# Kernel optimization log

Measured on AMD Instinct MI355X. Metric: run time of the kernel, lower is better.

## Reference

```python
import jax, jax.numpy as jnp
import numpy as np

TOP_K = 2

def setup_inputs() -> dict:
    key = jax.random.key(0)
    ks = jax.random.split(key, 5)
    B, T, C, E, H = 4, 2048, 1024, 16, 4096
    x = jax.random.normal(ks[0], (B, T, C), dtype=jnp.float32)
    w_router = jax.random.normal(ks[1], (C, E), dtype=jnp.float32) / np.sqrt(C)
    w1 = jax.random.normal(ks[2], (E, C, H), dtype=jnp.float32) / np.sqrt(C)
    b1 = jnp.zeros((E, H), dtype=jnp.float32)
    w2 = jax.random.normal(ks[3], (E, H, C), dtype=jnp.float32) / np.sqrt(H)
    b2 = jnp.zeros((E, C), dtype=jnp.float32)
    return {"x": x, "w_router": w_router, "w1": w1, "b1": b1, "w2": w2, "b2": b2}


def reference(x, w_router, w1, b1, w2, b2):
    B, T, C = x.shape
    E = w1.shape[0]
    xf = x.reshape(-1, C)                       # [N, C]
    N = xf.shape[0]

    logits = xf @ w_router                      # [N, E]
    rw, sel = jax.lax.top_k(logits, TOP_K)      # [N, K]
    rw = jax.nn.softmax(rw.astype(jnp.float32), axis=-1).astype(x.dtype)

    # combine weight per (token, expert): sum of routing weights over the
    # k-slots that selected that expert (equivalent to the per-k masked loop)
    comb = jnp.zeros((N, E), dtype=x.dtype)
    comb = comb.at[jnp.arange(N)[:, None], sel].add(rw)  # [N, E]

    # loop over experts via scan: out += comb[:, e:e+1] * FFN_e(xf)
    def step(acc, params):
        w1e, b1e, w2e, b2e, ce = params         # ce: [N]
        h = jax.nn.relu(xf @ w1e + b1e)         # [N, 4C]
        y = h @ w2e + b2e                       # [N, C]
        return acc + ce[:, None] * y, None

    out0 = jnp.zeros_like(xf)
    out, _ = jax.lax.scan(step, out0, (w1, b1, w2, b2, comb.T))
    return out.reshape(B, T, C)
```

## Files before the change

### kernel.cpp

```cpp
#include <hip/hip_runtime.h>
#include <hip/hip_bf16.h>


typedef __attribute__((ext_vector_type(4))) float f32x4;
typedef __attribute__((ext_vector_type(8))) __bf16 bf16x8;
typedef __attribute__((ext_vector_type(8))) unsigned short u16x8;

#define NEXP 16
#define CAP  2048
#define CDIM 1024
#define HDIM 4096
#define BM 128
#define BN 128
#define BK 64
#define KS2 2

__device__ __forceinline__ unsigned short f2bf(float f) {
  return __builtin_bit_cast(unsigned short, (__bf16)f);
}

__device__ __forceinline__ int swz(int row, int b) {
  return row * (BK * 2) + (b ^ (((row >> 1) & 7) << 4));
}

typedef __attribute__((address_space(3))) void  lds_void;
typedef __attribute__((address_space(1))) const void gbl_void;
__device__ __forceinline__ void gload16(const void* g, void* l) {
  __builtin_amdgcn_global_load_lds((gbl_void*)g, (lds_void*)l, 16, 0, 0);
}

__device__ __forceinline__ void xcd_remap(int& bx, int& by, int& bz) {
  const int gx = gridDim.x, gy = gridDim.y;
  const int nwg = gx * gy * gridDim.z;
  int flat = blockIdx.x + gx * (blockIdx.y + gy * blockIdx.z);
  flat = (flat & 7) * (nwg >> 3) + (flat >> 3);
  bx = flat % gx;
  const int t = flat / gx;
  by = t % gy;
  bz = t / gy;
}

__global__ __launch_bounds__(64) void router_kernel(
    const float* __restrict__ x, const float* __restrict__ wr,
    float* __restrict__ pair_w, int* __restrict__ counts,
    int* __restrict__ lists)
{
  const int n = blockIdx.x;
  const int l = threadIdx.x;
  const float* xrow = x + (size_t)n * CDIM;
  double acc[NEXP];
#pragma unroll
  for (int e = 0; e < NEXP; e++) acc[e] = 0.0;
  for (int it = 0; it < CDIM / 64; it++) {
    const int c = l + it * 64;
    const double xv = (double)xrow[c];
    const float* w = wr + c * NEXP;
#pragma unroll
    for (int e = 0; e < NEXP; e++) acc[e] += xv * (double)w[e];
  }
#pragma unroll
  for (int e = 0; e < NEXP; e++) {
    double v = acc[e];
    for (int off = 32; off > 0; off >>= 1) v += __shfl_xor(v, off, 64);
    acc[e] = v;
  }
  if (l == 0) {
    int e0 = 0; double b0 = acc[0];
    for (int e = 1; e < NEXP; e++) if (acc[e] > b0) { b0 = acc[e]; e0 = e; }
    int e1 = -1; double b1v = -1e300;
    for (int e = 0; e < NEXP; e++) {
      if (e == e0) continue;
      if (acc[e] > b1v) { b1v = acc[e]; e1 = e; }
    }
    const double d = exp(b1v - b0);
    pair_w[2 * n]     = (float)(1.0 / (1.0 + d));
    pair_w[2 * n + 1] = (float)(d / (1.0 + d));
    int p0 = atomicAdd(&counts[e0], 1);
    if (p0 < CAP) lists[e0 * CAP + p0] = 2 * n;
    int p1 = atomicAdd(&counts[e1], 1);
    if (p1 < CAP) lists[e1 * CAP + p1] = 2 * n + 1;
  }
}

__global__ __launch_bounds__(256) void cvt_x_kernel(
    const float* __restrict__ x, unsigned short* __restrict__ xb, int n8)
{
  const int i = blockIdx.x * 256 + threadIdx.x;
  if (i >= n8) return;
  float4 a = ((const float4*)x)[2 * i];
  float4 b = ((const float4*)x)[2 * i + 1];
  u16x8 v;
  v[0] = f2bf(a.x); v[1] = f2bf(a.y); v[2] = f2bf(a.z); v[3] = f2bf(a.w);
  v[4] = f2bf(b.x); v[5] = f2bf(b.y); v[6] = f2bf(b.z); v[7] = f2bf(b.w);
  ((u16x8*)xb)[i] = v;
}

__global__ __launch_bounds__(256) void transpose_cvt_kernel(
    const float* __restrict__ src, unsigned short* __restrict__ dst,
    int K, int Nn)
{
  __shared__ __align__(16) unsigned short tile[64][72];
  const size_t eoff = (size_t)blockIdx.z * K * Nn;
  const float* S = src + eoff;
  unsigned short* D = dst + eoff;
  const int n0 = blockIdx.x * 64, k0 = blockIdx.y * 64;
  const int t = threadIdx.x;
  {
    const int nl = (t & 15) * 4, kr = t >> 4;
#pragma unroll
    for (int p = 0; p < 4; p++) {
      const int k = kr + p * 16;
      float4 v = *(const float4*)(S + (size_t)(k0 + k) * Nn + n0 + nl);
      tile[nl + 0][k] = f2bf(v.x);
      tile[nl + 1][k] = f2bf(v.y);
      tile[nl + 2][k] = f2bf(v.z);
      tile[nl + 3][k] = f2bf(v.w);
    }
  }
  __syncthreads();
  {
    const int kq = (t & 7) * 8, nr = t >> 3;
#pragma unroll
    for (int p = 0; p < 2; p++) {
      const int n = nr + p * 32;
      u16x8 v = *(const u16x8*)&tile[n][kq];
      *(u16x8*)(D + (size_t)(n0 + n) * K + k0 + kq) = v;
    }
  }
}

__global__ __launch_bounds__(256) void gemm1_async_kernel(
    const unsigned short* __restrict__ xb, const unsigned short* __restrict__ wb,
    const float* __restrict__ b1, const int* __restrict__ counts,
    const int* __restrict__ lists, unsigned short* __restrict__ Hb)
{
  int bx, by, bz;
  xcd_remap(bx, by, bz);
  const int e = bz;
  int cnt = counts[e]; if (cnt > CAP) cnt = CAP;
  const int m0 = by * BM;
  if (m0 >= cnt) return;
  const int n0 = bx * BN;
  const int* list = lists + e * CAP;
  const unsigned short* W = wb + (size_t)e * CDIM * HDIM;

  __shared__ __align__(16) unsigned short As[BM * BK];
  __shared__ __align__(16) unsigned short Bs[BN * BK];

  const int t = threadIdx.x, wid = t >> 6, lane = t & 63;
  const char* ag[4]; const char* bg[4];
  unsigned short* al[4]; unsigned short* bl[4];
#pragma unroll
  for (int i = 0; i < 4; i++) {
    const int r = wid * 32 + i * 8 + (lane >> 3);
    const int cb = ((lane & 7) ^ ((r >> 1) & 7)) << 4;
    int ai = m0 + r; if (ai > cnt - 1) ai = cnt - 1;
    const int tok = list[ai] >> 1;
    ag[i] = (const char*)(xb + (size_t)tok * CDIM) + cb;
    bg[i] = (const char*)(W + (size_t)(n0 + r) * CDIM) + cb;
    al[i] = As + (wid * 32 + i * 8) * BK;
    bl[i] = Bs + (wid * 32 + i * 8) * BK;
  }

  const int wm = (wid >> 1) * 64, wn = (wid & 1) * 64;
  const int lrow = lane & 15, lgrp = lane >> 4;
  f32x4 acc[4][4] = {};

  for (int kt = 0; kt < CDIM; kt += BK) {
#pragma unroll
    for (int i = 0; i < 4; i++) {
      gload16(ag[i] + kt * 2, al[i]);
      gload16(bg[i] + kt * 2, bl[i]);
    }
    __syncthreads();
#pragma unroll
    for (int kk = 0; kk < 2; kk++) {
      bf16x8 af[4], bfr[4];
      const int kb = (kk * 32 + lgrp * 8) * 2;
#pragma unroll
      for (int i = 0; i < 4; i++)
        af[i] = *(const bf16x8*)((const char*)As + swz(wm + i * 16 + lrow, kb));
#pragma unroll
      for (int j = 0; j < 4; j++)
        bfr[j] = *(const bf16x8*)((const char*)Bs + swz(wn + j * 16 + lrow, kb));
#pragma unroll
      for (int i = 0; i < 4; i++)
#pragma unroll
        for (int j = 0; j < 4; j++)
          acc[i][j] = __builtin_amdgcn_mfma_f32_16x16x32_bf16(af[i], bfr[j], acc[i][j], 0, 0, 0);
    }
    __syncthreads();
  }

  int hrow[4][4]; bool valid[4][4];
#pragma unroll
  for (int i = 0; i < 4; i++)
#pragma unroll
    for (int r = 0; r < 4; r++) {
      const int mi = m0 + wm + i * 16 + lgrp * 4 + r;
      valid[i][r] = (mi < cnt);
      hrow[i][r] = list[valid[i][r] ? mi : (cnt - 1)];
    }
#pragma unroll
  for (int j = 0; j < 4; j++) {
    const int col = n0 + wn + j * 16 + lrow;
    const float bias = b1[e * HDIM + col];
#pragma unroll
    for (int i = 0; i < 4; i++)
#pragma unroll
      for (int r = 0; r < 4; r++)
        if (valid[i][r]) {
          float h = acc[i][j][r] + bias;
          h = h > 0.f ? h : 0.f;
          Hb[(size_t)hrow[i][r] * HDIM + col] = f2bf(h);
        }
  }
}

__global__ __launch_bounds__(256) void gemm2_async_kernel(
    const unsigned short* __restrict__ Hb, const unsigned short* __restrict__ wb,
    const float* __restrict__ b2, const float* __restrict__ pair_w,
    const int* __restrict__ counts, const int* __restrict__ lists,
    float* __restrict__ out)
{
  int bx, by, bz;
  xcd_remap(bx, by, bz);
  const int e = bz / KS2, ks = bz % KS2;
  int cnt = counts[e]; if (cnt > CAP) cnt = CAP;
  const int m0 = by * BM;
  if (m0 >= cnt) return;
  const int n0 = bx * BN;
  const int* list = lists + e * CAP;
  const unsigned short* W = wb + (size_t)e * HDIM * CDIM;
  const int kbeg = ks * (HDIM / KS2), kend = kbeg + HDIM / KS2;

  __shared__ __align__(16) unsigned short As[BM * BK];
  __shared__ __align__(16) unsigned short Bs[BN * BK];

  const int t = threadIdx.x, wid = t >> 6, lane = t & 63;
  const char* ag[4]; const char* bg[4];
  unsigned short* al[4]; unsigned short* bl[4];
#pragma unroll
  for (int i = 0; i < 4; i++) {
    const int r = wid * 32 + i * 8 + (lane >> 3);
    const int cb = ((lane & 7) ^ ((r >> 1) & 7)) << 4;
    int ai = m0 + r; if (ai > cnt - 1) ai = cnt - 1;
    const int pr = list[ai];
    ag[i] = (const char*)(Hb + (size_t)pr * HDIM) + cb;
    bg[i] = (const char*)(W + (size_t)(n0 + r) * HDIM) + cb;
    al[i] = As + (wid * 32 + i * 8) * BK;
    bl[i] = Bs + (wid * 32 + i * 8) * BK;
  }

  const int wm = (wid >> 1) * 64, wn = (wid & 1) * 64;
  const int lrow = lane & 15, lgrp = lane >> 4;
  f32x4 acc[4][4] = {};

  for (int kt = kbeg; kt < kend; kt += BK) {
#pragma unroll
    for (int i = 0; i < 4; i++) {
      gload16(ag[i] + kt * 2, al[i]);
      gload16(bg[i] + kt * 2, bl[i]);
    }
    __syncthreads();
#pragma unroll
    for (int kk = 0; kk < 2; kk++) {
      bf16x8 af[4], bfr[4];
      const int kb = (kk * 32 + lgrp * 8) * 2;
#pragma unroll
      for (int i = 0; i < 4; i++)
        af[i] = *(const bf16x8*)((const char*)As + swz(wm + i * 16 + lrow, kb));
#pragma unroll
      for (int j = 0; j < 4; j++)
        bfr[j] = *(const bf16x8*)((const char*)Bs + swz(wn + j * 16 + lrow, kb));
#pragma unroll
      for (int i = 0; i < 4; i++)
#pragma unroll
        for (int j = 0; j < 4; j++)
          acc[i][j] = __builtin_amdgcn_mfma_f32_16x16x32_bf16(af[i], bfr[j], acc[i][j], 0, 0, 0);
    }
    __syncthreads();
  }

  float wgt[4][4]; int tok[4][4]; bool valid[4][4];
#pragma unroll
  for (int i = 0; i < 4; i++)
#pragma unroll
    for (int r = 0; r < 4; r++) {
      const int mi = m0 + wm + i * 16 + lgrp * 4 + r;
      valid[i][r] = (mi < cnt);
      const int p = list[valid[i][r] ? mi : (cnt - 1)];
      wgt[i][r] = pair_w[p];
      tok[i][r] = p >> 1;
    }
#pragma unroll
  for (int j = 0; j < 4; j++) {
    const int col = n0 + wn + j * 16 + lrow;
    const float bias = (ks == 0) ? b2[e * CDIM + col] : 0.f;
#pragma unroll
    for (int i = 0; i < 4; i++)
#pragma unroll
      for (int r = 0; r < 4; r++)
        if (valid[i][r])
          atomicAdd(out + (size_t)tok[i][r] * CDIM + col,
                    wgt[i][r] * (acc[i][j][r] + bias));
  }
}

__global__ __launch_bounds__(256) void gemm1_f32_kernel(
    const float* __restrict__ x, const float* __restrict__ w1,
    const float* __restrict__ b1, const int* __restrict__ counts,
    const int* __restrict__ lists, unsigned short* __restrict__ Hb,
    int e_base, int h_by_pair)
{
  const int e = e_base + blockIdx.z;
  int cnt = counts[e]; if (cnt > CAP) cnt = CAP;
  const int m0 = blockIdx.y * BM;
  if (m0 >= cnt) return;
  const int n0 = blockIdx.x * BN;
  const int* list = lists + e * CAP;
  const float* W = w1 + (size_t)e * CDIM * HDIM;
  __shared__ __align__(16) unsigned short As[BM * BK];
  __shared__ __align__(16) unsigned short Bs[BN * BK];
  const int t = threadIdx.x;
  const int a_row = t >> 1, a_half = t & 1;
  int a_idx = m0 + a_row; if (a_idx > cnt - 1) a_idx = cnt - 1;
  const float* a_src = x + (size_t)(list[a_idx] >> 1) * CDIM + a_half * 32;
  const int b_np = t & 63, b_kg = t >> 6;
  const int wid = t >> 6, lane = t & 63;
  const int wm = (wid >> 1) * 64, wn = (wid & 1) * 64;
  const int lrow = lane & 15, lgrp = lane >> 4;
  f32x4 acc[4][4] = {};
  for (int kt = 0; kt < CDIM; kt += BK) {
    {
      const float* s = a_src + kt;
      u16x8 cv[4];
#pragma unroll
      for (int q = 0; q < 4; q++) {
        float4 v0 = *(const float4*)(s + q * 8);
        float4 v1 = *(const float4*)(s + q * 8 + 4);
        cv[q][0] = f2bf(v0.x); cv[q][1] = f2bf(v0.y);
        cv[q][2] = f2bf(v0.z); cv[q][3] = f2bf(v0.w);
        cv[q][4] = f2bf(v1.x); cv[q][5] = f2bf(v1.y);
        cv[q][6] = f2bf(v1.z); cv[q][7] = f2bf(v1.w);
      }
#pragma unroll
      for (int q = 0; q < 4; q++)
        *(u16x8*)((char*)As + swz(a_row, (a_half * 32 + q * 8) * 2)) = cv[q];
    }
    {
#pragma unroll
      for (int it = 0; it < 2; it++) {
        const int k0 = (b_kg + 4 * it) * 8;
        u16x8 c0, c1;
#pragma unroll
        for (int j = 0; j < 8; j++) {
          float2 v = *(const float2*)(W + (size_t)(kt + k0 + j) * HDIM + n0 + 2 * b_np);
          c0[j] = f2bf(v.x); c1[j] = f2bf(v.y);
        }
        *(u16x8*)((char*)Bs + swz(2 * b_np,     k0 * 2)) = c0;
        *(u16x8*)((char*)Bs + swz(2 * b_np + 1, k0 * 2)) = c1;
      }
    }
    __syncthreads();
#pragma unroll
    for (int kk = 0; kk < 2; kk++) {
      bf16x8 af[4], bfr[4];
      const int kb = (kk * 32 + lgrp * 8) * 2;
#pragma unroll
      for (int i = 0; i < 4; i++)
        af[i] = *(const bf16x8*)((const char*)As + swz(wm + i * 16 + lrow, kb));
#pragma unroll
      for (int j = 0; j < 4; j++)
        bfr[j] = *(const bf16x8*)((const char*)Bs + swz(wn + j * 16 + lrow, kb));
#pragma unroll
      for (int i = 0; i < 4; i++)
#pragma unroll
        for (int j = 0; j < 4; j++)
          acc[i][j] = __builtin_amdgcn_mfma_f32_16x16x32_bf16(af[i], bfr[j], acc[i][j], 0, 0, 0);
    }
    __syncthreads();
  }
  int hrow[4][4]; bool valid[4][4];
#pragma unroll
  for (int i = 0; i < 4; i++)
#pragma unroll
    for (int r = 0; r < 4; r++) {
      const int mi = m0 + wm + i * 16 + lgrp * 4 + r;
      valid[i][r] = (mi < cnt);
      const int idx = valid[i][r] ? mi : (cnt - 1);
      hrow[i][r] = h_by_pair ? list[idx] : idx;
    }
#pragma unroll
  for (int j = 0; j < 4; j++) {
    const int col = n0 + wn + j * 16 + lrow;
    const float bias = b1[e * HDIM + col];
#pragma unroll
    for (int i = 0; i < 4; i++)
#pragma unroll
      for (int r = 0; r < 4; r++)
        if (valid[i][r]) {
          float h = acc[i][j][r] + bias;
          h = h > 0.f ? h : 0.f;
          Hb[(size_t)hrow[i][r] * HDIM + col] = f2bf(h);
        }
  }
}

__global__ __launch_bounds__(256) void gemm2_f32_kernel(
    const unsigned short* __restrict__ Hb, const float* __restrict__ w2,
    const float* __restrict__ b2, const float* __restrict__ pair_w,
    const int* __restrict__ counts, const int* __restrict__ lists,
    float* __restrict__ out, int e_base, int h_by_pair)
{
  const int e = e_base + blockIdx.z;
  int cnt = counts[e]; if (cnt > CAP) cnt = CAP;
  const int m0 = blockIdx.y * BM;
  if (m0 >= cnt) return;
  const int n0 = blockIdx.x * BN;
  const int* list = lists + e * CAP;
  const float* W = w2 + (size_t)e * HDIM * CDIM;
  __shared__ __align__(16) unsigned short As[BM * BK];
  __shared__ __align__(16) unsigned short Bs[BN * BK];
  const int t = threadIdx.x;
  const int a_row = t >> 1, a_half = t & 1;
  int a_idx = m0 + a_row; if (a_idx > cnt - 1) a_idx = cnt - 1;
  const unsigned short* a_src =
      Hb + (size_t)(h_by_pair ? list[a_idx] : a_idx) * HDIM + a_half * 32;
  const int b_np = t & 63, b_kg = t >> 6;
  const int wid = t >> 6, lane = t & 63;
  const int wm = (wid >> 1) * 64, wn = (wid & 1) * 64;
  const int lrow = lane & 15, lgrp = lane >> 4;
  f32x4 acc[4][4] = {};
  for (int kt = 0; kt < HDIM; kt += BK) {
    {
      const unsigned short* s = a_src + kt;
#pragma unroll
      for (int q = 0; q < 4; q++) {
        u16x8 v = *(const u16x8*)(s + q * 8);
        *(u16x8*)((char*)As + swz(a_row, (a_half * 32 + q * 8) * 2)) = v;
      }
    }
    {
#pragma unroll
      for (int it = 0; it < 2; it++) {
        const int k0 = (b_kg + 4 * it) * 8;
        u16x8 c0, c1;
#pragma unroll
        for (int j = 0; j < 8; j++) {
          float2 v = *(const float2*)(W + (size_t)(kt + k0 + j) * CDIM + n0 + 2 * b_np);
          c0[j] = f2bf(v.x); c1[j] = f2bf(v.y);
        }
        *(u16x8*)((char*)Bs + swz(2 * b_np,     k0 * 2)) = c0;
        *(u16x8*)((char*)Bs + swz(2 * b_np + 1, k0 * 2)) = c1;
      }
    }
    __syncthreads();
#pragma unroll
    for (int kk = 0; kk < 2; kk++) {
      bf16x8 af[4], bfr[4];
      const int kb = (kk * 32 + lgrp * 8) * 2;
#pragma unroll
      for (int i = 0; i < 4; i++)
        af[i] = *(const bf16x8*)((const char*)As + swz(wm + i * 16 + lrow, kb));
#pragma unroll
      for (int j = 0; j < 4; j++)
        bfr[j] = *(const bf16x8*)((const char*)Bs + swz(wn + j * 16 + lrow, kb));
#pragma unroll
      for (int i = 0; i < 4; i++)
#pragma unroll
        for (int j = 0; j < 4; j++)
          acc[i][j] = __builtin_amdgcn_mfma_f32_16x16x32_bf16(af[i], bfr[j], acc[i][j], 0, 0, 0);
    }
    __syncthreads();
  }
  float wgt[4][4]; int tok[4][4]; bool valid[4][4];
#pragma unroll
  for (int i = 0; i < 4; i++)
#pragma unroll
    for (int r = 0; r < 4; r++) {
      const int mi = m0 + wm + i * 16 + lgrp * 4 + r;
      valid[i][r] = (mi < cnt);
      const int idx = valid[i][r] ? mi : (cnt - 1);
      const int p = list[idx];
      wgt[i][r] = pair_w[p];
      tok[i][r] = p >> 1;
    }
#pragma unroll
  for (int j = 0; j < 4; j++) {
    const int col = n0 + wn + j * 16 + lrow;
    const float bias = b2[e * CDIM + col];
#pragma unroll
    for (int i = 0; i < 4; i++)
#pragma unroll
      for (int r = 0; r < 4; r++)
        if (valid[i][r])
          atomicAdd(out + (size_t)tok[i][r] * CDIM + col,
                    wgt[i][r] * (acc[i][j][r] + bias));
  }
}

extern "C" void kernel_launch(void* const* d_in, const int* in_sizes, int n_in,
                              void* d_out, int out_size, void* d_ws, size_t ws_size,
                              hipStream_t stream)
{
  const float* x  = (const float*)d_in[0];
  const float* wr = (const float*)d_in[1];
  const float* w1 = (const float*)d_in[2];
  const float* b1 = (const float*)d_in[3];
  const float* w2 = (const float*)d_in[4];
  const float* b2 = (const float*)d_in[5];
  float* out = (float*)d_out;

  const int N = in_sizes[0] / CDIM;

  char* ws = (char*)d_ws;
  int* counts = (int*)ws;
  int* lists  = (int*)(ws + 256);
  float* pw   = (float*)(ws + 256 + NEXP * CAP * 4);
  size_t off = 256 + (size_t)NEXP * CAP * 4 + (size_t)2 * N * 4;
  off = (off + 255) & ~(size_t)255;
  unsigned short* xb = (unsigned short*)(ws + off);
  const size_t xb_sz = (size_t)N * CDIM * 2;
  unsigned short* Hb = (unsigned short*)(ws + off + xb_sz);
  const size_t Hb_sz = (size_t)2 * N * HDIM * 2;
  unsigned short* wb = (unsigned short*)(ws + off + xb_sz + Hb_sz);
  const size_t wb_sz = (size_t)NEXP * CDIM * HDIM * 2;

  const size_t need_new = off + xb_sz + Hb_sz + wb_sz;
  const size_t need_old = off + Hb_sz;

  hipMemsetAsync(d_ws, 0, 64, stream);
  hipMemsetAsync(d_out, 0, (size_t)out_size * 4, stream);

  router_kernel<<<N, 64, 0, stream>>>(x, wr, pw, counts, lists);

  if (ws_size >= need_new) {
    cvt_x_kernel<<<(N * CDIM / 8 + 255) / 256, 256, 0, stream>>>(
        x, xb, N * CDIM / 8);
    transpose_cvt_kernel<<<dim3(HDIM / 64, CDIM / 64, NEXP), 256, 0, stream>>>(
        w1, wb, CDIM, HDIM);
    gemm1_async_kernel<<<dim3(HDIM / BN, CAP / BM, NEXP), 256, 0, stream>>>(
        xb, wb, b1, counts, lists, Hb);
    transpose_cvt_kernel<<<dim3(CDIM / 64, HDIM / 64, NEXP), 256, 0, stream>>>(
        w2, wb, HDIM, CDIM);
    gemm2_async_kernel<<<dim3(CDIM / BN, CAP / BM, NEXP * KS2), 256, 0, stream>>>(
        Hb, wb, b2, pw, counts, lists, out);
  } else if (ws_size >= need_old) {
    unsigned short* Hb0 = (unsigned short*)(ws + off);
    gemm1_f32_kernel<<<dim3(HDIM / BN, CAP / BM, NEXP), 256, 0, stream>>>(
        x, w1, b1, counts, lists, Hb0, 0, 1);
    gemm2_f32_kernel<<<dim3(CDIM / BN, CAP / BM, NEXP), 256, 0, stream>>>(
        Hb0, w2, b2, pw, counts, lists, out, 0, 1);
  }
}
```

Before: 1.088 ms.

## Double-buffer LDS tiles in async GEMM kernels to overlap loads with MFMA

The async bf16 GEMM kernels now keep two LDS buffers for the A and B tiles. Each iteration issues the global-to-LDS loads for the next K tile before computing the current one, then uses a partial vmcnt wait plus raw s_barrier in place of two __syncthreads. The goal is to hide global memory latency behind MFMA work. This doubles LDS use per block to 64KB, which may reduce occupancy, and it depends on the hand-written waitcnt counts being correct.

```diff
diff --git a/kernel.cpp b/kernel.cpp
--- a/kernel.cpp
+++ b/kernel.cpp
@@ -14,6 +14,7 @@
 #define BN 128
 #define BK 64
 #define KS2 2
+#define TILE_E (BM * BK)
 
 __device__ __forceinline__ unsigned short f2bf(float f) {
   return __builtin_bit_cast(unsigned short, (__bf16)f);
@@ -129,6 +130,25 @@
   }
 }
 
+#define MFMA_COMPUTE(Abase, Bbase)                                             \
+  _Pragma("unroll")                                                            \
+  for (int kk = 0; kk < 2; kk++) {                                             \
+    bf16x8 af[4], bfr[4];                                                      \
+    const int kb = (kk * 32 + lgrp * 8) * 2;                                   \
+    _Pragma("unroll")                                                          \
+    for (int i = 0; i < 4; i++)                                                \
+      af[i] = *(const bf16x8*)((Abase) + swz(wm + i * 16 + lrow, kb));         \
+    _Pragma("unroll")                                                          \
+    for (int j = 0; j < 4; j++)                                                \
+      bfr[j] = *(const bf16x8*)((Bbase) + swz(wn + j * 16 + lrow, kb));        \
+    _Pragma("unroll")                                                          \
+    for (int i = 0; i < 4; i++)                                                \
+      _Pragma("unroll")                                                        \
+      for (int j = 0; j < 4; j++)                                              \
+        acc[i][j] = __builtin_amdgcn_mfma_f32_16x16x32_bf16(                   \
+            af[i], bfr[j], acc[i][j], 0, 0, 0);                                \
+  }
+
 __global__ __launch_bounds__(256) void gemm1_async_kernel(
     const unsigned short* __restrict__ xb, const unsigned short* __restrict__ wb,
     const float* __restrict__ b1, const int* __restrict__ counts,
@@ -144,8 +164,8 @@
   const int* list = lists + e * CAP;
   const unsigned short* W = wb + (size_t)e * CDIM * HDIM;
 
-  __shared__ __align__(16) unsigned short As[BM * BK];
-  __shared__ __align__(16) unsigned short Bs[BN * BK];
+  __shared__ __align__(16) unsigned short As[2 * TILE_E];
+  __shared__ __align__(16) unsigned short Bs[2 * TILE_E];
 
   const int t = threadIdx.x, wid = t >> 6, lane = t & 63;
   const char* ag[4]; const char* bg[4];
@@ -166,30 +186,34 @@
   const int lrow = lane & 15, lgrp = lane >> 4;
   f32x4 acc[4][4] = {};
 
-  for (int kt = 0; kt < CDIM; kt += BK) {
+#pragma unroll
+  for (int i = 0; i < 4; i++) {
+    gload16(ag[i], al[i]);
+    gload16(bg[i], bl[i]);
+  }
+  const int NT = CDIM / BK;
+  for (int tt = 0; tt < NT - 1; ++tt) {
+    const int p = tt & 1;
+    const int koff = (tt + 1) * (BK * 2);
 #pragma unroll
     for (int i = 0; i < 4; i++) {
-      gload16(ag[i] + kt * 2, al[i]);
-      gload16(bg[i] + kt * 2, bl[i]);
-    }
-    __syncthreads();
-#pragma unroll
-    for (int kk = 0; kk < 2; kk++) {
-      bf16x8 af[4], bfr[4];
-      const int kb = (kk * 32 + lgrp * 8) * 2;
-#pragma unroll
-      for (int i = 0; i < 4; i++)
-        af[i] = *(const bf16x8*)((const char*)As + swz(wm + i * 16 + lrow, kb));
-#pragma unroll
-      for (int j = 0; j < 4; j++)
-        bfr[j] = *(const bf16x8*)((const char*)Bs + swz(wn + j * 16 + lrow, kb));
-#pragma unroll
-      for (int i = 0; i < 4; i++)
-#pragma unroll
-        for (int j = 0; j < 4; j++)
-          acc[i][j] = __builtin_amdgcn_mfma_f32_16x16x32_bf16(af[i], bfr[j], acc[i][j], 0, 0, 0);
-    }
-    __syncthreads();
+      gload16(ag[i] + koff, al[i] + (p ^ 1) * TILE_E);
+      gload16(bg[i] + koff, bl[i] + (p ^ 1) * TILE_E);
+    }
+    asm volatile("s_waitcnt vmcnt(8)" ::: "memory");
+    asm volatile("s_barrier" ::: "memory");
+    const char* Ab = (const char*)As + p * (TILE_E * 2);
+    const char* Bb = (const char*)Bs + p * (TILE_E * 2);
+    MFMA_COMPUTE(Ab, Bb)
+    asm volatile("s_barrier" ::: "memory");
+  }
+  {
+    const int p = (NT - 1) & 1;
+    asm volatile("s_waitcnt vmcnt(0)" ::: "memory");
+    asm volatile("s_barrier" ::: "memory");
+    const char* Ab = (const char*)As + p * (TILE_E * 2);
+    const char* Bb = (const char*)Bs + p * (TILE_E * 2);
+    MFMA_COMPUTE(Ab, Bb)
   }
 
   int hrow[4][4]; bool valid[4][4];
@@ -232,10 +256,10 @@
   const int n0 = bx * BN;
   const int* list = lists + e * CAP;
   const unsigned short* W = wb + (size_t)e * HDIM * CDIM;
-  const int kbeg = ks * (HDIM / KS2), kend = kbeg + HDIM / KS2;
-
-  __shared__ __align__(16) unsigned short As[BM * BK];
-  __shared__ __align__(16) unsigned short Bs[BN * BK];
+  const int kbeg = ks * (HDIM / KS2);
+
+  __shared__ __align__(16) unsigned short As[2 * TILE_E];
+  __shared__ __align__(16) unsigned short Bs[2 * TILE_E];
 
   const int t = threadIdx.x, wid = t >> 6, lane = t & 63;
   const char* ag[4]; const char* bg[4];
@@ -246,8 +270,8 @@
     const int cb = ((lane & 7) ^ ((r >> 1) & 7)) << 4;
     int ai = m0 + r; if (ai > cnt - 1) ai = cnt - 1;
     const int pr = list[ai];
-    ag[i] = (const char*)(Hb + (size_t)pr * HDIM) + cb;
-    bg[i] = (const char*)(W + (size_t)(n0 + r) * HDIM) + cb;
+    ag[i] = (const char*)(Hb + (size_t)pr * HDIM + kbeg) + cb;
+    bg[i] = (const char*)(W + (size_t)(n0 + r) * HDIM + kbeg) + cb;
     al[i] = As + (wid * 32 + i * 8) * BK;
     bl[i] = Bs + (wid * 32 + i * 8) * BK;
   }
@@ -256,30 +280,34 @@
   const int lrow = lane & 15, lgrp = lane >> 4;
   f32x4 acc[4][4] = {};
 
-  for (int kt = kbeg; kt < kend; kt += BK) {
+#pragma unroll
+  for (int i = 0; i < 4; i++) {
+    gload16(ag[i], al[i]);
+    gload16(bg[i], bl[i]);
+  }
+  const int NT = (HDIM / KS2) / BK;
+  for (int tt = 0; tt < NT - 1; ++tt) {
+    const int p = tt & 1;
+    const int koff = (tt + 1) * (BK * 2);
 #pragma unroll
     for (int i = 0; i < 4; i++) {
-      gload16(ag[i] + kt * 2, al[i]);
-      gload16(bg[i] + kt * 2, bl[i]);
-    }
-    __syncthreads();
-#pragma unroll
-    for (int kk = 0; kk < 2; kk++) {
-      bf16x8 af[4], bfr[4];
-      const int kb = (kk * 32 + lgrp * 8) * 2;
-#pragma unroll
-      for (int i = 0; i < 4; i++)
-        af[i] = *(const bf16x8*)((const char*)As + swz(wm + i * 16 + lrow, kb));
-#pragma unroll
-      for (int j = 0; j < 4; j++)
-        bfr[j] = *(const bf16x8*)((const char*)Bs + swz(wn + j * 16 + lrow, kb));
-#pragma unroll
-      for (int i = 0; i < 4; i++)
-#pragma unroll
-        for (int j = 0; j < 4; j++)
-          acc[i][j] = __builtin_amdgcn_mfma_f32_16x16x32_bf16(af[i], bfr[j], acc[i][j], 0, 0, 0);
-    }
-    __syncthreads();
+      gload16(ag[i] + koff, al[i] + (p ^ 1) * TILE_E);
+      gload16(bg[i] + koff, bl[i] + (p ^ 1) * TILE_E);
+    }
+    asm volatile("s_waitcnt vmcnt(8)" ::: "memory");
+    asm volatile("s_barrier" ::: "memory");
+    const char* Ab = (const char*)As + p * (TILE_E * 2);
+    const char* Bb = (const char*)Bs + p * (TILE_E * 2);
+    MFMA_COMPUTE(Ab, Bb)
+    asm volatile("s_barrier" ::: "memory");
+  }
+  {
+    const int p = (NT - 1) & 1;
+    asm volatile("s_waitcnt vmcnt(0)" ::: "memory");
+    asm volatile("s_barrier" ::: "memory");
+    const char* Ab = (const char*)As + p * (TILE_E * 2);
+    const char* Bb = (const char*)Bs + p * (TILE_E * 2);
+    MFMA_COMPUTE(Ab, Bb)
   }
 
   float wgt[4][4]; int tok[4][4]; bool valid[4][4];
@@ -320,8 +348,8 @@
   const int n0 = blockIdx.x * BN;
   const int* list = lists + e * CAP;
   const float* W = w1 + (size_t)e * CDIM * HDIM;
-  __shared__ __align__(16) unsigned short As[BM * BK];
-  __shared__ __align__(16) unsigned short Bs[BN * BK];
+  __shared__ __align__(16) unsigned short As[TILE_E];
+  __shared__ __align__(16) unsigned short Bs[TILE_E];
   const int t = threadIdx.x;
   const int a_row = t >> 1, a_half = t & 1;
   int a_idx = m0 + a_row; if (a_idx > cnt - 1) a_idx = cnt - 1;
@@ -363,22 +391,7 @@
       }
     }
     __syncthreads();
-#pragma unroll
-    for (int kk = 0; kk < 2; kk++) {
-      bf16x8 af[4], bfr[4];
-      const int kb = (kk * 32 + lgrp * 8) * 2;
-#pragma unroll
-      for (int i = 0; i < 4; i++)
-        af[i] = *(const bf16x8*)((const char*)As + swz(wm + i * 16 + lrow, kb));
-#pragma unroll
-      for (int j = 0; j < 4; j++)
-        bfr[j] = *(const bf16x8*)((const char*)Bs + swz(wn + j * 16 + lrow, kb));
-#pragma unroll
-      for (int i = 0; i < 4; i++)
-#pragma unroll
-        for (int j = 0; j < 4; j++)
-          acc[i][j] = __builtin_amdgcn_mfma_f32_16x16x32_bf16(af[i], bfr[j], acc[i][j], 0, 0, 0);
-    }
+    MFMA_COMPUTE((const char*)As, (const char*)Bs)
     __syncthreads();
   }
   int hrow[4][4]; bool valid[4][4];
@@ -420,8 +433,8 @@
   const int n0 = blockIdx.x * BN;
   const int* list = lists + e * CAP;
   const float* W = w2 + (size_t)e * HDIM * CDIM;
-  __shared__ __align__(16) unsigned short As[BM * BK];
-  __shared__ __align__(16) unsigned short Bs[BN * BK];
+  __shared__ __align__(16) unsigned short As[TILE_E];
+  __shared__ __align__(16) unsigned short Bs[TILE_E];
   const int t = threadIdx.x;
   const int a_row = t >> 1, a_half = t & 1;
   int a_idx = m0 + a_row; if (a_idx > cnt - 1) a_idx = cnt - 1;
@@ -456,22 +469,7 @@
       }
     }
     __syncthreads();
-#pragma unroll
-    for (int kk = 0; kk < 2; kk++) {
-      bf16x8 af[4], bfr[4];
-      const int kb = (kk * 32 + lgrp * 8) * 2;
-#pragma unroll
-      for (int i = 0; i < 4; i++)
-        af[i] = *(const bf16x8*)((const char*)As + swz(wm + i * 16 + lrow, kb));
-#pragma unroll
-      for (int j = 0; j < 4; j++)
-        bfr[j] = *(const bf16x8*)((const char*)Bs + swz(wn + j * 16 + lrow, kb));
-#pragma unroll
-      for (int i = 0; i < 4; i++)
-#pragma unroll
-        for (int j = 0; j < 4; j++)
-          acc[i][j] = __builtin_amdgcn_mfma_f32_16x16x32_bf16(af[i], bfr[j], acc[i][j], 0, 0, 0);
-    }
+    MFMA_COMPUTE((const char*)As, (const char*)Bs)
     __syncthreads();
   }
   float wgt[4][4]; int tok[4][4]; bool valid[4][4];
```

New measurement: 1.078 ms. Within noise of the previous version (-0.9%).
